# Kernel tuning notes

Measured on AMD Instinct MI355X. Metric: run time of the kernel, lower is better.

## Reference

```python
import jax, jax.numpy as jnp
import numpy as np

B, T, C, H = 4, 2048, 2048, 16
HD = C // H  # head_size = 128
EPS = 1e-5


def layernorm(x, g, b):
    mu = jnp.mean(x, axis=-1, keepdims=True)
    var = jnp.var(x, axis=-1, keepdims=True)
    return (x - mu) * jax.lax.rsqrt(var + EPS) * g + b


def setup_inputs() -> dict:
    key = jax.random.key(0)
    ks = jax.random.split(key, 12)
    s_attn = 1.0 / np.sqrt(C)
    s_ffn1 = 1.0 / np.sqrt(C)
    s_ffn2 = 1.0 / np.sqrt(4 * C)
    return {
        "x": jax.random.normal(ks[0], (B, T, C), jnp.float32),
        "Wq": jax.random.normal(ks[1], (H, C, HD), jnp.float32) * s_attn,
        "Wk": jax.random.normal(ks[2], (H, C, HD), jnp.float32) * s_attn,
        "Wv": jax.random.normal(ks[3], (H, C, HD), jnp.float32) * s_attn,
        "Wp": jax.random.normal(ks[4], (C, C), jnp.float32) * s_attn,
        "bp": jnp.zeros((C,), jnp.float32),
        "W1": jax.random.normal(ks[5], (C, 4 * C), jnp.float32) * s_ffn1,
        "b1": jnp.zeros((4 * C,), jnp.float32),
        "W2": jax.random.normal(ks[6], (4 * C, C), jnp.float32) * s_ffn2,
        "b2": jnp.zeros((C,), jnp.float32),
        "g1": jnp.ones((C,), jnp.float32),
        "beta1": jnp.zeros((C,), jnp.float32),
        "g2": jnp.ones((C,), jnp.float32),
        "beta2": jnp.zeros((C,), jnp.float32),
    }


def reference(x, Wq, Wk, Wv, Wp, bp, W1, b1, W2, b2, g1, beta1, g2, beta2):
    # --- attention sublayer (pre-LN, causal) ---
    h = layernorm(x, g1, beta1)
    q = jnp.einsum("btc,hcd->bhtd", h, Wq)
    k = jnp.einsum("bsc,hcd->bhsd", h, Wk)
    v = jnp.einsum("bsc,hcd->bhsd", h, Wv)
    scores = jnp.einsum("bhtd,bhsd->bhts", q, k) / jnp.sqrt(jnp.asarray(HD, x.dtype))
    causal = jnp.tril(jnp.ones((T, T), bool))
    scores = jnp.where(causal, scores, jnp.asarray(-jnp.inf, x.dtype))
    w = jax.nn.softmax(scores, axis=-1)  # dropout = identity (eval mode)
    o = jnp.einsum("bhts,bhsd->bhtd", w, v)
    o = o.transpose(0, 2, 1, 3).reshape(B, T, C)  # concat heads
    x = x + o @ Wp + bp
    # --- feed-forward sublayer ---
    h2 = layernorm(x, g2, beta2)
    f = jax.nn.gelu(h2 @ W1 + b1, approximate=False)
    x = x + f @ W2 + b2
    return x
```

## Files before the change

kernel.cpp:

```cpp
#include <hip/hip_runtime.h>
#include <math.h>

#define B_ 4
#define T_ 2048
#define C_ 2048
#define H_ 16
#define HD_ 128

typedef __attribute__((ext_vector_type(8))) short short8;
typedef __attribute__((ext_vector_type(4))) float f32x4;
typedef unsigned short u16;
typedef unsigned int u32;

__device__ __forceinline__ u16 f2bf(float f) {
  union { float f; unsigned u; } v; v.f = f;
  unsigned r = v.u + 0x7FFFu + ((v.u >> 16) & 1u);
  return (u16)(r >> 16);
}

__device__ __forceinline__ void gld16(const void* g, void* l) {
  __builtin_amdgcn_global_load_lds(
      (__attribute__((address_space(1))) void*)(void*)g,
      (__attribute__((address_space(3))) void*)l, 16, 0, 0);
}

__global__ __launch_bounds__(256) void tconv(const float* __restrict__ in,
                                             u16* __restrict__ out,
                                             int K, int N,
                                             long inBS, long outBS) {
  __shared__ float tile[32][33];
  const float* inb = in + (long)blockIdx.z * inBS;
  u16* outb = out + (long)blockIdx.z * outBS;
  int k0 = blockIdx.x << 5, n0 = blockIdx.y << 5;
  int t = threadIdx.x;
  {
    int kk = t >> 3, nn = (t & 7) << 2;
    float4 v = *(const float4*)(inb + (long)(k0 + kk) * N + n0 + nn);
    tile[kk][nn + 0] = v.x; tile[kk][nn + 1] = v.y;
    tile[kk][nn + 2] = v.z; tile[kk][nn + 3] = v.w;
  }
  __syncthreads();
  {
    int nn = t >> 3, kk = (t & 7) << 2;
    ushort4 o;
    o.x = f2bf(tile[kk + 0][nn]); o.y = f2bf(tile[kk + 1][nn]);
    o.z = f2bf(tile[kk + 2][nn]); o.w = f2bf(tile[kk + 3][nn]);
    *(ushort4*)(outb + (long)(n0 + nn) * K + k0 + kk) = o;
  }
}

__global__ __launch_bounds__(256) void ln_rows(const float* __restrict__ x,
                                               const float* __restrict__ gam,
                                               const float* __restrict__ bet,
                                               u16* __restrict__ out) {
  int row = blockIdx.x;
  const float* xr = x + (size_t)row * C_;
  int t = threadIdx.x;
  float4 v0 = *(const float4*)(xr + t * 8);
  float4 v1 = *(const float4*)(xr + t * 8 + 4);
  float s = v0.x + v0.y + v0.z + v0.w + v1.x + v1.y + v1.z + v1.w;
  float ss = v0.x * v0.x + v0.y * v0.y + v0.z * v0.z + v0.w * v0.w +
             v1.x * v1.x + v1.y * v1.y + v1.z * v1.z + v1.w * v1.w;
  for (int d = 32; d > 0; d >>= 1) {
    s += __shfl_down(s, d);
    ss += __shfl_down(ss, d);
  }
  __shared__ float red[8];
  int wv = t >> 6;
  if ((t & 63) == 0) { red[wv] = s; red[4 + wv] = ss; }
  __syncthreads();
  s = red[0] + red[1] + red[2] + red[3];
  ss = red[4] + red[5] + red[6] + red[7];
  float mu = s * (1.0f / C_);
  float var = ss * (1.0f / C_) - mu * mu;
  float rs = rsqrtf(var + 1e-5f);
  int c = t * 8;
  float vv[8] = {v0.x, v0.y, v0.z, v0.w, v1.x, v1.y, v1.z, v1.w};
  ushort4 o0, o1;
  o0.x = f2bf((vv[0] - mu) * rs * gam[c + 0] + bet[c + 0]);
  o0.y = f2bf((vv[1] - mu) * rs * gam[c + 1] + bet[c + 1]);
  o0.z = f2bf((vv[2] - mu) * rs * gam[c + 2] + bet[c + 2]);
  o0.w = f2bf((vv[3] - mu) * rs * gam[c + 3] + bet[c + 3]);
  o1.x = f2bf((vv[4] - mu) * rs * gam[c + 4] + bet[c + 4]);
  o1.y = f2bf((vv[5] - mu) * rs * gam[c + 5] + bet[c + 5]);
  o1.z = f2bf((vv[6] - mu) * rs * gam[c + 6] + bet[c + 6]);
  o1.w = f2bf((vv[7] - mu) * rs * gam[c + 7] + bet[c + 7]);
  *(ushort4*)(out + (size_t)row * C_ + c) = o0;
  *(ushort4*)(out + (size_t)row * C_ + c + 4) = o1;
}

template <int EPI>
__global__ __launch_bounds__(512, 2) void gemm256(
    const u16* __restrict__ A, const u16* __restrict__ BT,
    int M, int N, int K, int lda, int ldb,
    u16* __restrict__ oq, u16* __restrict__ ok, u16* __restrict__ ovt,
    float* __restrict__ of32, const float* __restrict__ resid,
    const float* __restrict__ bias, u16* __restrict__ obf, int addBias) {
  extern __shared__ char smem[];
  int nbx = N >> 8;
  int nwg = gridDim.x;
  int flat = blockIdx.x;
  int sw = (flat & 7) * (nwg >> 3) + (flat >> 3);
  int bx = sw % nbx, by = sw / nbx;
  int m0 = by << 8, n0 = bx << 8;
  int tid = threadIdx.x;
  int lane = tid & 63, wave = tid >> 6;
  int wm = wave >> 2, wn = wave & 3;
  int l15 = lane & 15, l16 = lane >> 4;
  int nt = K >> 6;

  f32x4 acc[8][4] = {};
  short8 af[4][2], bf[4][2];

  auto stage = [&](int b, int r, int k0) {
    int row = (r & 3) * 64 + (tid >> 3);
    int lslot = (tid & 7) ^ (row & 7);
    char* dst = smem + ((r < 4) ? 0 : 65536) + b * 32768 + (r & 3) * 8192 + tid * 16;
    const u16* src = ((r < 4) ? (A + (long)(m0 + row) * lda)
                              : (BT + (long)(n0 + row) * ldb)) +
                     k0 + lslot * 8;
    gld16(src, dst);
  };
  auto ldA = [&](int cur, int mf, int kk) {
    int row = wm * 128 + mf * 16 + l15;
    int slot = (kk * 4 + l16) ^ (row & 7);
    return *(const short8*)(smem + cur * 32768 + row * 128 + slot * 16);
  };
  auto ldB = [&](int cur, int nf, int kk) {
    int row = wn * 64 + nf * 16 + l15;
    int slot = (kk * 4 + l16) ^ (row & 7);
    return *(const short8*)(smem + 65536 + cur * 32768 + row * 128 + slot * 16);
  };

#pragma unroll
  for (int r = 0; r < 8; ++r) stage(0, r, 0);

  for (int t = 0; t < nt; ++t) {
    int cur = t & 1, nxt = cur ^ 1;
    bool more = (t + 1) < nt;
    int k1 = (t + 1) << 6;
    if (more) {
      stage(nxt, 0, k1); stage(nxt, 1, k1); stage(nxt, 2, k1);
      asm volatile("s_waitcnt vmcnt(3)" ::: "memory");
    } else {
      asm volatile("s_waitcnt vmcnt(0)" ::: "memory");
    }
    __builtin_amdgcn_s_barrier();
#pragma unroll
    for (int mq = 0; mq < 4; ++mq)
#pragma unroll
      for (int kk = 0; kk < 2; ++kk) af[mq][kk] = ldA(cur, mq, kk);
#pragma unroll
    for (int nq = 0; nq < 2; ++nq)
#pragma unroll
      for (int kk = 0; kk < 2; ++kk) bf[nq][kk] = ldB(cur, nq, kk);
    if (more) { stage(nxt, 3, k1); stage(nxt, 4, k1); stage(nxt, 5, k1); }
    __builtin_amdgcn_s_barrier();
    asm volatile("s_waitcnt lgkmcnt(0)" ::: "memory");
    __builtin_amdgcn_s_setprio(1);
#pragma unroll
    for (int mq = 0; mq < 4; ++mq)
#pragma unroll
      for (int nq = 0; nq < 2; ++nq)
#pragma unroll
        for (int kk = 0; kk < 2; ++kk)
          acc[mq][nq] = __builtin_amdgcn_mfma_f32_16x16x32_bf16(
              af[mq][kk], bf[nq][kk], acc[mq][nq], 0, 0, 0);
    __builtin_amdgcn_s_setprio(0);
    __builtin_amdgcn_s_barrier();
#pragma unroll
    for (int nq = 2; nq < 4; ++nq)
#pragma unroll
      for (int kk = 0; kk < 2; ++kk) bf[nq][kk] = ldB(cur, nq, kk);
    if (more) { stage(nxt, 6, k1); stage(nxt, 7, k1); }
    __builtin_amdgcn_s_barrier();
    asm volatile("s_waitcnt lgkmcnt(0)" ::: "memory");
    __builtin_amdgcn_s_setprio(1);
#pragma unroll
    for (int mq = 0; mq < 4; ++mq)
#pragma unroll
      for (int nq = 2; nq < 4; ++nq)
#pragma unroll
        for (int kk = 0; kk < 2; ++kk)
          acc[mq][nq] = __builtin_amdgcn_mfma_f32_16x16x32_bf16(
              af[mq][kk], bf[nq][kk], acc[mq][nq], 0, 0, 0);
    __builtin_amdgcn_s_setprio(0);
    __builtin_amdgcn_s_barrier();
#pragma unroll
    for (int mq = 0; mq < 4; ++mq)
#pragma unroll
      for (int kk = 0; kk < 2; ++kk) af[mq][kk] = ldA(cur, 4 + mq, kk);
    __builtin_amdgcn_s_barrier();
    asm volatile("s_waitcnt lgkmcnt(0)" ::: "memory");
    __builtin_amdgcn_s_setprio(1);
#pragma unroll
    for (int mq = 0; mq < 4; ++mq)
#pragma unroll
      for (int nq = 0; nq < 2; ++nq)
#pragma unroll
        for (int kk = 0; kk < 2; ++kk)
          acc[4 + mq][nq] = __builtin_amdgcn_mfma_f32_16x16x32_bf16(
              af[mq][kk], bf[nq][kk], acc[4 + mq][nq], 0, 0, 0);
    __builtin_amdgcn_s_setprio(0);
    __builtin_amdgcn_s_barrier();
    __builtin_amdgcn_s_setprio(1);
#pragma unroll
    for (int mq = 0; mq < 4; ++mq)
#pragma unroll
      for (int nq = 2; nq < 4; ++nq)
#pragma unroll
        for (int kk = 0; kk < 2; ++kk)
          acc[4 + mq][nq] = __builtin_amdgcn_mfma_f32_16x16x32_bf16(
              af[mq][kk], bf[nq][kk], acc[4 + mq][nq], 0, 0, 0);
    __builtin_amdgcn_s_setprio(0);
    __builtin_amdgcn_s_barrier();
  }

#pragma unroll
  for (int mf = 0; mf < 8; ++mf) {
#pragma unroll
    for (int nf = 0; nf < 4; ++nf) {
      int rowf = m0 + wm * 128 + mf * 16 + l16 * 4;
      int col = n0 + wn * 64 + nf * 16 + l15;
      if constexpr (EPI == 0) {
        int seg = col >> 11, cn = col & 2047;
        int hh = cn >> 7, dd = cn & 127;
        int bb = rowf >> 11, t0 = rowf & 2047;
        if (seg == 2) {
          ushort4 o;
          o.x = f2bf(acc[mf][nf][0]); o.y = f2bf(acc[mf][nf][1]);
          o.z = f2bf(acc[mf][nf][2]); o.w = f2bf(acc[mf][nf][3]);
          *(ushort4*)(ovt + ((long)(bb * H_ + hh) * HD_ + dd) * T_ + t0) = o;
        } else {
          u16* dst = (seg == 0) ? oq : ok;
#pragma unroll
          for (int r = 0; r < 4; ++r)
            dst[((long)(bb * H_ + hh) * T_ + t0 + r) * HD_ + dd] =
                f2bf(acc[mf][nf][r]);
        }
      } else if constexpr (EPI == 1) {
#pragma unroll
        for (int r = 0; r < 4; ++r) {
          long idx = (long)(rowf + r) * N + col;
          of32[idx] = resid[idx] + bias[col] + acc[mf][nf][r];
        }
      } else if constexpr (EPI == 2) {
#pragma unroll
        for (int r = 0; r < 4; ++r) {
          float v = acc[mf][nf][r] + bias[col];
          float g = 0.5f * v * (1.0f + erff(v * 0.70710678118654752f));
          obf[(long)(rowf + r) * N + col] = f2bf(g);
        }
      } else {
#pragma unroll
        for (int r = 0; r < 4; ++r) {
          long idx = (long)(rowf + r) * N + col;
          float v = acc[mf][nf][r];
          if (addBias) v += bias[col];
          of32[idx] += v;
        }
      }
    }
  }
}

__global__ __launch_bounds__(256) void attn_fwd(const u16* __restrict__ q,
                                                const u16* __restrict__ k,
                                                const u16* __restrict__ vt,
                                                u16* __restrict__ o) {
  extern __shared__ char asmem[];
  int bid = blockIdx.x;
  int bh = bid & 63;
  int qb = 31 - (bid >> 6);
  int q0 = qb << 6;
  int tid = threadIdx.x, lane = tid & 63, wave = tid >> 6;
  int l15 = lane & 15, l16 = lane >> 4;
  int wq0 = q0 + wave * 16;
  const u16* kbase = k + (long)bh * T_ * HD_;
  const u16* vbase = vt + (long)bh * HD_ * T_;
  char* Psw = asmem + 65536 + wave * 2048;

  short8 qf[4];
#pragma unroll
  for (int kk = 0; kk < 4; ++kk)
    qf[kk] = *(const short8*)(q + ((long)bh * T_ + wq0 + l15) * HD_ +
                              kk * 32 + l16 * 8);

  f32x4 accO[8] = {};
  float m_r[4], l_r[4];
#pragma unroll
  for (int r = 0; r < 4; ++r) { m_r[r] = -INFINITY; l_r[r] = 0.f; }
  const float sc = 0.08838834764831845f * 1.4426950408889634f;

  int nt = qb + 1;

  auto stage = [&](int b, int t) {
    int s0 = t << 6;
    char* Kd = asmem + b * 16384;
    char* Vd = asmem + 32768 + b * 16384;
#pragma unroll
    for (int r = 0; r < 4; ++r) {
      int off = r * 4096 + tid * 16;
      int krow = off >> 8;
      int kslot = (tid & 15) ^ (krow & 7);
      gld16(kbase + (long)(s0 + krow) * HD_ + kslot * 8, Kd + off);
      int dd = off >> 7;
      int vslot = (tid & 7) ^ (dd & 7);
      gld16(vbase + (long)dd * T_ + s0 + vslot * 8, Vd + off);
    }
  };

  stage(0, 0);
  asm volatile("s_waitcnt vmcnt(0)" ::: "memory");
  __syncthreads();

  for (int t = 0; t < nt; ++t) {
    int s0 = t << 6;
    int cur = t & 1;
    bool more = (t + 1 < nt);
    if (more) stage(cur ^ 1, t + 1);

    if (s0 <= wq0 + 15) {
      const char* Kc = asmem + cur * 16384;
      const char* Vc = asmem + 32768 + cur * 16384;
      bool needmask = (s0 + 63 > wq0);
      f32x4 S[4];
#pragma unroll
      for (int sb = 0; sb < 4; ++sb) {
        f32x4 s = {};
#pragma unroll
        for (int kk = 0; kk < 4; ++kk) {
          int srow = sb * 16 + l15;
          int kb = srow * 256 + (((kk * 4 + l16) ^ (srow & 7)) << 4);
          short8 kf = *(const short8*)(Kc + kb);
          s = __builtin_amdgcn_mfma_f32_16x16x32_bf16(qf[kk], kf, s, 0, 0, 0);
        }
        S[sb] = s;
      }
      float mxl[4];
      bool growL = false;
#pragma unroll
      for (int r = 0; r < 4; ++r) {
        int tt = wq0 + 4 * l16 + r;
        float mx = -INFINITY;
#pragma unroll
        for (int sb = 0; sb < 4; ++sb) {
          float v = S[sb][r] * sc;
          if (needmask && (s0 + sb * 16 + l15 > tt)) v = -INFINITY;
          S[sb][r] = v;
          mx = fmaxf(mx, v);
        }
        mxl[r] = mx;
        growL = growL || (mx > m_r[r] + 8.0f);
      }
      bool anyg = __any(growL);
      float al[4];
      if (anyg) {
#pragma unroll
        for (int r = 0; r < 4; ++r) {
          float mx = mxl[r];
          mx = fmaxf(mx, __shfl_xor(mx, 1));
          mx = fmaxf(mx, __shfl_xor(mx, 2));
          mx = fmaxf(mx, __shfl_xor(mx, 4));
          mx = fmaxf(mx, __shfl_xor(mx, 8));
          float mo = m_r[r];
          float mn = fmaxf(mo, mx);
          al[r] = exp2f(mo - mn);
          m_r[r] = mn;
        }
      } else {
#pragma unroll
        for (int r = 0; r < 4; ++r) al[r] = 1.0f;
      }
#pragma unroll
      for (int r = 0; r < 4; ++r) {
        float mn = m_r[r];
        int prow = 4 * l16 + r;
        float rs = 0.f;
#pragma unroll
        for (int sb = 0; sb < 4; ++sb) {
          float p = exp2f(S[sb][r] - mn);
          rs += p;
          int pb = (prow * 128 + (sb * 16 + l15) * 2) ^ ((prow & 7) << 4);
          *(u16*)(Psw + pb) = f2bf(p);
        }
        rs += __shfl_xor(rs, 1);
        rs += __shfl_xor(rs, 2);
        rs += __shfl_xor(rs, 4);
        rs += __shfl_xor(rs, 8);
        l_r[r] = l_r[r] * al[r] + rs;
      }
      if (anyg) {
#pragma unroll
        for (int db = 0; db < 8; ++db)
#pragma unroll
          for (int r = 0; r < 4; ++r) accO[db][r] *= al[r];
      }
      short8 pf[2];
#pragma unroll
      for (int st = 0; st < 2; ++st) {
        int prow = l15;
        int pb = (prow * 128 + (st * 4 + l16) * 16) ^ ((prow & 7) << 4);
        pf[st] = *(const short8*)(Psw + pb);
      }
#pragma unroll
      for (int db = 0; db < 8; ++db) {
#pragma unroll
        for (int st = 0; st < 2; ++st) {
          int vrow = db * 16 + l15;
          int vb = (vrow * 128 + (st * 4 + l16) * 16) ^ ((vrow & 7) << 4);
          short8 vf = *(const short8*)(Vc + vb);
          accO[db] = __builtin_amdgcn_mfma_f32_16x16x32_bf16(pf[st], vf,
                                                             accO[db], 0, 0, 0);
        }
      }
    }
    if (more) asm volatile("s_waitcnt vmcnt(0)" ::: "memory");
    __syncthreads();
  }

  int bb = bh >> 4, hh = bh & 15;
  float inv[4];
#pragma unroll
  for (int r = 0; r < 4; ++r) inv[r] = 1.0f / l_r[r];
#pragma unroll
  for (int db = 0; db < 8; ++db)
#pragma unroll
    for (int r = 0; r < 4; ++r) {
      int tt = wq0 + 4 * l16 + r;
      o[((long)bb * T_ + tt) * C_ + hh * HD_ + db * 16 + l15] =
          f2bf(accO[db][r] * inv[r]);
    }
}

extern "C" void kernel_launch(void* const* d_in, const int* in_sizes, int n_in,
                              void* d_out, int out_size, void* d_ws, size_t ws_size,
                              hipStream_t stream) {
  (void)in_sizes; (void)n_in; (void)out_size; (void)ws_size;
  const float* x   = (const float*)d_in[0];
  const float* Wq  = (const float*)d_in[1];
  const float* Wk  = (const float*)d_in[2];
  const float* Wv  = (const float*)d_in[3];
  const float* Wp  = (const float*)d_in[4];
  const float* bp  = (const float*)d_in[5];
  const float* W1  = (const float*)d_in[6];
  const float* b1  = (const float*)d_in[7];
  const float* W2  = (const float*)d_in[8];
  const float* b2  = (const float*)d_in[9];
  const float* g1  = (const float*)d_in[10];
  const float* be1 = (const float*)d_in[11];
  const float* g2  = (const float*)d_in[12];
  const float* be2 = (const float*)d_in[13];
  float* out = (float*)d_out;

  (void)hipFuncSetAttribute((const void*)gemm256<0>,
                            hipFuncAttributeMaxDynamicSharedMemorySize, 131072);
  (void)hipFuncSetAttribute((const void*)gemm256<1>,
                            hipFuncAttributeMaxDynamicSharedMemorySize, 131072);
  (void)hipFuncSetAttribute((const void*)gemm256<2>,
                            hipFuncAttributeMaxDynamicSharedMemorySize, 131072);
  (void)hipFuncSetAttribute((const void*)gemm256<3>,
                            hipFuncAttributeMaxDynamicSharedMemorySize, 131072);
  (void)hipFuncSetAttribute((const void*)attn_fwd,
                            hipFuncAttributeMaxDynamicSharedMemorySize, 73728);

  char* ws = (char*)d_ws;
  size_t off = 0;
  auto alloc = [&](size_t n) {
    void* p = ws + off;
    off += (n + 255) & ~(size_t)255;
    return p;
  };
  u16* wqkvT = (u16*)alloc((size_t)6144 * 2048 * 2);
  u16* wpT   = (u16*)alloc((size_t)2048 * 2048 * 2);
  u16* w1T   = (u16*)alloc((size_t)8192 * 2048 * 2);
  u16* w2T   = (u16*)alloc((size_t)2048 * 8192 * 2);
  u16* hb    = (u16*)alloc((size_t)8192 * 2048 * 2);
  u16* qbuf  = (u16*)alloc((size_t)8192 * 2048 * 2);
  u16* kbuf  = (u16*)alloc((size_t)8192 * 2048 * 2);
  u16* vtbuf = (u16*)alloc((size_t)8192 * 2048 * 2);
  u16* ob = hb;
  u16* fb = qbuf;

  tconv<<<dim3(64, 4, 16), 256, 0, stream>>>(Wq, wqkvT, 2048, 128,
                                             (long)2048 * 128, (long)128 * 2048);
  tconv<<<dim3(64, 4, 16), 256, 0, stream>>>(Wk, wqkvT + (size_t)2048 * 2048, 2048, 128,
                                             (long)2048 * 128, (long)128 * 2048);
  tconv<<<dim3(64, 4, 16), 256, 0, stream>>>(Wv, wqkvT + (size_t)4096 * 2048, 2048, 128,
                                             (long)2048 * 128, (long)128 * 2048);
  tconv<<<dim3(64, 64, 1), 256, 0, stream>>>(Wp, wpT, 2048, 2048, 0, 0);
  tconv<<<dim3(64, 256, 1), 256, 0, stream>>>(W1, w1T, 2048, 8192, 0, 0);
  tconv<<<dim3(256, 64, 1), 256, 0, stream>>>(W2, w2T, 8192, 2048, 0, 0);

  ln_rows<<<8192, 256, 0, stream>>>(x, g1, be1, hb);
  gemm256<0><<<768, 512, 131072, stream>>>(hb, wqkvT, 8192, 6144, 2048, 2048, 2048,
                                           qbuf, kbuf, vtbuf, nullptr, nullptr,
                                           nullptr, nullptr, 0);
  attn_fwd<<<2048, 256, 73728, stream>>>(qbuf, kbuf, vtbuf, ob);
  gemm256<1><<<256, 512, 131072, stream>>>(ob, wpT, 8192, 2048, 2048, 2048, 2048,
                                           nullptr, nullptr, nullptr, out, x, bp,
                                           nullptr, 0);

  ln_rows<<<8192, 256, 0, stream>>>(out, g2, be2, hb);
  for (int c = 0; c < 2; ++c) {
    gemm256<2><<<512, 512, 131072, stream>>>(hb, w1T + (size_t)c * 4096 * 2048,
                                             8192, 4096, 2048, 2048, 2048,
                                             nullptr, nullptr, nullptr, nullptr,
                                             nullptr, b1 + c * 4096, fb, 0);
    gemm256<3><<<256, 512, 131072, stream>>>(fb, w2T + (size_t)c * 4096,
                                             8192, 2048, 4096, 4096, 8192,
                                             nullptr, nullptr, nullptr, out,
                                             nullptr, b2, nullptr, c == 0 ? 1 : 0);
  }
}
```

Measured before the change: 1.142 ms.

## Double-buffer GEMM register fragments and collapse per-phase barriers into one sync

Splits the A and B register fragments into two sets so the next quarter-tile's LDS reads can overlap the current MFMA block. It issues all eight global-to-LDS stage loads for the next K-tile at the start of the iteration, replacing the staggered loads and partial vmcnt waits. The many per-phase s_barrier calls are replaced by a single __syncthreads at the end of each K step, after which the first fragments of the next tile are prefetched. The aim is to cut barrier stalls and LDS-read latency in the main loop. In exchange it uses more VGPRs and does a full wait on the global loads once per tile instead of partial waits.

```diff
diff --git a/kernel.cpp b/kernel.cpp
--- a/kernel.cpp
+++ b/kernel.cpp
@@ -110,7 +110,7 @@
   int nt = K >> 6;
 
   f32x4 acc[8][4] = {};
-  short8 af[4][2], bf[4][2];
+  short8 afA[4][2], afB[4][2], bfA[2][2], bfB[2][2];
 
   auto stage = [&](int b, int r, int k0) {
     int row = (r & 3) * 64 + (tid >> 3);
@@ -134,29 +134,29 @@
 
 #pragma unroll
   for (int r = 0; r < 8; ++r) stage(0, r, 0);
+  __syncthreads();
+
+#pragma unroll
+  for (int mq = 0; mq < 4; ++mq)
+#pragma unroll
+    for (int kk = 0; kk < 2; ++kk) afA[mq][kk] = ldA(0, mq, kk);
+#pragma unroll
+  for (int nq = 0; nq < 2; ++nq)
+#pragma unroll
+    for (int kk = 0; kk < 2; ++kk) bfA[nq][kk] = ldB(0, nq, kk);
 
   for (int t = 0; t < nt; ++t) {
     int cur = t & 1, nxt = cur ^ 1;
     bool more = (t + 1) < nt;
     int k1 = (t + 1) << 6;
     if (more) {
-      stage(nxt, 0, k1); stage(nxt, 1, k1); stage(nxt, 2, k1);
-      asm volatile("s_waitcnt vmcnt(3)" ::: "memory");
-    } else {
-      asm volatile("s_waitcnt vmcnt(0)" ::: "memory");
+#pragma unroll
+      for (int r = 0; r < 8; ++r) stage(nxt, r, k1);
     }
-    __builtin_amdgcn_s_barrier();
-#pragma unroll
-    for (int mq = 0; mq < 4; ++mq)
-#pragma unroll
-      for (int kk = 0; kk < 2; ++kk) af[mq][kk] = ldA(cur, mq, kk);
 #pragma unroll
     for (int nq = 0; nq < 2; ++nq)
 #pragma unroll
-      for (int kk = 0; kk < 2; ++kk) bf[nq][kk] = ldB(cur, nq, kk);
-    if (more) { stage(nxt, 3, k1); stage(nxt, 4, k1); stage(nxt, 5, k1); }
-    __builtin_amdgcn_s_barrier();
-    asm volatile("s_waitcnt lgkmcnt(0)" ::: "memory");
+      for (int kk = 0; kk < 2; ++kk) bfB[nq][kk] = ldB(cur, 2 + nq, kk);
     __builtin_amdgcn_s_setprio(1);
 #pragma unroll
     for (int mq = 0; mq < 4; ++mq)
@@ -165,33 +165,22 @@
 #pragma unroll
         for (int kk = 0; kk < 2; ++kk)
           acc[mq][nq] = __builtin_amdgcn_mfma_f32_16x16x32_bf16(
-              af[mq][kk], bf[nq][kk], acc[mq][nq], 0, 0, 0);
+              afA[mq][kk], bfA[nq][kk], acc[mq][nq], 0, 0, 0);
     __builtin_amdgcn_s_setprio(0);
-    __builtin_amdgcn_s_barrier();
-#pragma unroll
-    for (int nq = 2; nq < 4; ++nq)
-#pragma unroll
-      for (int kk = 0; kk < 2; ++kk) bf[nq][kk] = ldB(cur, nq, kk);
-    if (more) { stage(nxt, 6, k1); stage(nxt, 7, k1); }
-    __builtin_amdgcn_s_barrier();
-    asm volatile("s_waitcnt lgkmcnt(0)" ::: "memory");
+#pragma unroll
+    for (int mq = 0; mq < 4; ++mq)
+#pragma unroll
+      for (int kk = 0; kk < 2; ++kk) afB[mq][kk] = ldA(cur, 4 + mq, kk);
     __builtin_amdgcn_s_setprio(1);
 #pragma unroll
     for (int mq = 0; mq < 4; ++mq)
 #pragma unroll
-      for (int nq = 2; nq < 4; ++nq)
+      for (int nq = 0; nq < 2; ++nq)
 #pragma unroll
         for (int kk = 0; kk < 2; ++kk)
-          acc[mq][nq] = __builtin_amdgcn_mfma_f32_16x16x32_bf16(
-              af[mq][kk], bf[nq][kk], acc[mq][nq], 0, 0, 0);
+          acc[mq][2 + nq] = __builtin_amdgcn_mfma_f32_16x16x32_bf16(
+              afA[mq][kk], bfB[nq][kk], acc[mq][2 + nq], 0, 0, 0);
     __builtin_amdgcn_s_setprio(0);
-    __builtin_amdgcn_s_barrier();
-#pragma unroll
-    for (int mq = 0; mq < 4; ++mq)
-#pragma unroll
-      for (int kk = 0; kk < 2; ++kk) af[mq][kk] = ldA(cur, 4 + mq, kk);
-    __builtin_amdgcn_s_barrier();
-    asm volatile("s_waitcnt lgkmcnt(0)" ::: "memory");
     __builtin_amdgcn_s_setprio(1);
 #pragma unroll
     for (int mq = 0; mq < 4; ++mq)
@@ -200,20 +189,29 @@
 #pragma unroll
         for (int kk = 0; kk < 2; ++kk)
           acc[4 + mq][nq] = __builtin_amdgcn_mfma_f32_16x16x32_bf16(
-              af[mq][kk], bf[nq][kk], acc[4 + mq][nq], 0, 0, 0);
+              afB[mq][kk], bfA[nq][kk], acc[4 + mq][nq], 0, 0, 0);
     __builtin_amdgcn_s_setprio(0);
-    __builtin_amdgcn_s_barrier();
     __builtin_amdgcn_s_setprio(1);
 #pragma unroll
     for (int mq = 0; mq < 4; ++mq)
 #pragma unroll
-      for (int nq = 2; nq < 4; ++nq)
+      for (int nq = 0; nq < 2; ++nq)
 #pragma unroll
         for (int kk = 0; kk < 2; ++kk)
-          acc[4 + mq][nq] = __builtin_amdgcn_mfma_f32_16x16x32_bf16(
-              af[mq][kk], bf[nq][kk], acc[4 + mq][nq], 0, 0, 0);
+          acc[4 + mq][2 + nq] = __builtin_amdgcn_mfma_f32_16x16x32_bf16(
+              afB[mq][kk], bfB[nq][kk], acc[4 + mq][2 + nq], 0, 0, 0);
     __builtin_amdgcn_s_setprio(0);
-    __builtin_amdgcn_s_barrier();
+    if (more) {
+      __syncthreads();
+#pragma unroll
+      for (int mq = 0; mq < 4; ++mq)
+#pragma unroll
+        for (int kk = 0; kk < 2; ++kk) afA[mq][kk] = ldA(nxt, mq, kk);
+#pragma unroll
+      for (int nq = 0; nq < 2; ++nq)
+#pragma unroll
+        for (int kk = 0; kk < 2; ++kk) bfA[nq][kk] = ldB(nxt, nq, kk);
+    }
   }
 
 #pragma unroll
```

Result: faster. 1.113 ms (-2.5%).
